# Kernel tuning notes

Measured on AMD Instinct MI355X. Metric: run time of the kernel, lower is better.

## Reference

```python
import jax, jax.numpy as jnp
import numpy as np
from jax import lax

N = 500_000
D = 128            # in_channels
B = 8192           # number of graphs (segments)
T = 6              # processing_steps


def setup_inputs() -> dict:
    key = jax.random.key(0)
    k1, k2, k3, k4, k5, k6 = jax.random.split(key, 6)
    x = jax.random.normal(k1, (N, D), dtype=jnp.float32)
    batch = jnp.sort(jax.random.randint(k2, (N,), 0, B)).astype(jnp.int64)
    s = 1.0 / np.sqrt(D)  # torch LSTM init scale: U(-1/sqrt(hidden), 1/sqrt(hidden))
    W_ih = jax.random.uniform(k3, (4 * D, 2 * D), jnp.float32, -s, s)
    W_hh = jax.random.uniform(k4, (4 * D, D), jnp.float32, -s, s)
    b_ih = jax.random.uniform(k5, (4 * D,), jnp.float32, -s, s)
    b_hh = jax.random.uniform(k6, (4 * D,), jnp.float32, -s, s)
    return {"x": x, "batch": batch, "W_ih": W_ih, "W_hh": W_hh,
            "b_ih": b_ih, "b_hh": b_hh}


def reference(x, batch, W_ih, W_hh, b_ih, b_hh):
    d = x.shape[1]
    h0 = jnp.zeros((B, d), x.dtype)
    c0 = jnp.zeros((B, d), x.dtype)
    q_star0 = jnp.zeros((B, 2 * d), x.dtype)

    def step(carry, _):
        h, c, q_star = carry
        # single-layer torch LSTM cell on seq of length 1
        gates = q_star @ W_ih.T + b_ih + h @ W_hh.T + b_hh  # [B, 4d]
        i, f, g, o = jnp.split(gates, 4, axis=-1)
        i = jax.nn.sigmoid(i)
        f = jax.nn.sigmoid(f)
        g = jnp.tanh(g)
        o = jax.nn.sigmoid(o)
        c = f * c + i * g
        h = o * jnp.tanh(c)
        q = h  # [B, d]
        # attention logits per node
        e = jnp.sum(x * q[batch], axis=-1)  # [N]
        # segment-wise stable softmax (PyG softmax semantics)
        e_max = jax.ops.segment_max(e, batch, num_segments=B)
        ex = jnp.exp(e - e_max[batch])
        denom = jax.ops.segment_sum(ex, batch, num_segments=B)
        a = ex / (denom[batch] + 1e-16)  # [N]
        # scatter-add readout
        r = jax.ops.segment_sum(a[:, None] * x, batch, num_segments=B)  # [B, d]
        q_star = jnp.concatenate([q, r], axis=-1)
        return (h, c, q_star), None

    (h, c, q_star), _ = lax.scan(step, (h0, c0, q_star0), None, length=T)
    return q_star
```

## Files before the change

kernel.cpp:

```cpp
#include <hip/hip_runtime.h>
#include <hip/hip_bf16.h>
#include <cstddef>
#include <cstdint>

#define NNODES 500000
#define DIM    128
#define NSEG   8192
#define TSTEPS 6
#define WCHUNK 32

typedef __attribute__((ext_vector_type(8))) short bf16x8;
typedef __attribute__((ext_vector_type(4))) float f32x4;
typedef unsigned short ushort_t;

static __device__ inline ushort_t f2bf_u(float f) {
    __hip_bfloat16 h = __float2bfloat16(f);
    return *reinterpret_cast<ushort_t*>(&h);
}
static __device__ inline float bfu2f(ushort_t u) {
    union { unsigned i; float f; } c; c.i = ((unsigned)u) << 16; return c.f;
}
#define LGKM_WAIT() __asm__ __volatile__("s_waitcnt lgkmcnt(0)" ::: "memory")

__global__ void seg_bounds_k(const int* __restrict__ batch, int* __restrict__ seg, int n) {
    int b = blockIdx.x * blockDim.x + threadIdx.x;
    if (b > NSEG) return;
    int lo = 0, hi = n;
    while (lo < hi) {
        int mid = (lo + hi) >> 1;
        if (batch[mid] < b) lo = mid + 1; else hi = mid;
    }
    seg[b] = lo;
}

__global__ __launch_bounds__(256) void wconv_k(
    const float* __restrict__ Wih, const float* __restrict__ Whh,
    __hip_bfloat16* __restrict__ wbuf)
{
    int idx = blockIdx.x * 256 + threadIdx.x;
    int n = idx / 384, k = idx - n * 384;
    float v = (k < 256) ? Wih[n * 256 + k] : Whh[n * 128 + (k - 256)];
    wbuf[idx] = __float2bfloat16(v);
}

__global__ __launch_bounds__(256) void gemm_mfma_k(
    const __hip_bfloat16* __restrict__ abuf,
    const __hip_bfloat16* __restrict__ wbuf,
    float* __restrict__ gates)
{
    __shared__ char As[128 * 128];
    __shared__ char Bs[64 * 128];
    const int tid  = threadIdx.x;
    const int lane = tid & 63, wave = tid >> 6;
    const int wrow = (wave >> 1) * 64;
    const int wcol = (wave & 1) * 32;
    const int m0 = blockIdx.y * 128;
    const int n0 = blockIdx.x * 64;

    const int ar  = tid >> 1;
    const int acb = (tid & 1) * 64;
    const int br  = tid >> 2;
    const int bcb = (tid & 3) * 32;

    const char* aP = (const char*)(abuf + (size_t)(m0 + ar) * 384) + acb;
    const char* bP = (const char*)(wbuf + (size_t)(n0 + br) * 384) + bcb;

    f32x4 acc[4][2] = {};

    int4 ra[4]; int4 rb2[2];
    #pragma unroll
    for (int c = 0; c < 4; ++c) ra[c]  = *(const int4*)(aP + c * 16);
    #pragma unroll
    for (int c = 0; c < 2; ++c) rb2[c] = *(const int4*)(bP + c * 16);

    char* asw = As + ar * 128;
    char* bsw = Bs + br * 128;
    const int amask = (ar & 7) << 4;
    const int bmask = (br & 7) << 4;

    for (int s = 0; s < 6; ++s) {
        __syncthreads();
        #pragma unroll
        for (int c = 0; c < 4; ++c)
            *(int4*)(asw + ((acb + c * 16) ^ amask)) = ra[c];
        #pragma unroll
        for (int c = 0; c < 2; ++c)
            *(int4*)(bsw + ((bcb + c * 16) ^ bmask)) = rb2[c];
        __syncthreads();

        if (s < 5) {
            const char* aN = aP + (size_t)(s + 1) * 128;
            const char* bN = bP + (size_t)(s + 1) * 128;
            #pragma unroll
            for (int c = 0; c < 4; ++c) ra[c]  = *(const int4*)(aN + c * 16);
            #pragma unroll
            for (int c = 0; c < 2; ++c) rb2[c] = *(const int4*)(bN + c * 16);
        }

        #pragma unroll
        for (int ks = 0; ks < 2; ++ks) {
            const int kb = ks * 64 + ((lane >> 4) << 4);
            bf16x8 af[4], bfr[2];
            #pragma unroll
            for (int rbk = 0; rbk < 4; ++rbk) {
                int r = wrow + rbk * 16 + (lane & 15);
                af[rbk] = *(const bf16x8*)(As + r * 128 + (kb ^ ((r & 7) << 4)));
            }
            #pragma unroll
            for (int cb = 0; cb < 2; ++cb) {
                int n = wcol + cb * 16 + (lane & 15);
                bfr[cb] = *(const bf16x8*)(Bs + n * 128 + (kb ^ ((n & 7) << 4)));
            }
            #pragma unroll
            for (int rbk = 0; rbk < 4; ++rbk)
                #pragma unroll
                for (int cb = 0; cb < 2; ++cb)
                    acc[rbk][cb] = __builtin_amdgcn_mfma_f32_16x16x32_bf16(
                        af[rbk], bfr[cb], acc[rbk][cb], 0, 0, 0);
        }
    }

    const int rowb = (lane >> 4) << 2;
    const int coll = lane & 15;
    #pragma unroll
    for (int rbk = 0; rbk < 4; ++rbk)
        #pragma unroll
        for (int cb = 0; cb < 2; ++cb) {
            int row = m0 + wrow + rbk * 16 + rowb;
            int col = n0 + wcol + cb * 16 + coll;
            float* gp = gates + (size_t)row * 512 + col;
            #pragma unroll
            for (int reg = 0; reg < 4; ++reg)
                gp[(size_t)reg * 512] = acc[rbk][cb][reg];
        }
}

__global__ __launch_bounds__(128) void attn_lstm_k(
    const float* __restrict__ x, ushort_t* __restrict__ xbf,
    const int* __restrict__ seg, const float* __restrict__ gates,
    const float* __restrict__ bih, const float* __restrict__ bhh,
    float* __restrict__ cbuf, float* __restrict__ qstar,
    __hip_bfloat16* __restrict__ abuf,
    int t0, int read_bf, int write_bf)
{
    const int tid  = threadIdx.x;
    const int wv   = tid >> 6, lane = tid & 63;
    const int b    = blockIdx.x;
    const int l16  = lane & 15, grp = lane >> 4;

    __shared__ ushort_t xs[2][WCHUNK * 128];
    __shared__ float    es[2][WCHUNK];
    __shared__ float    mstat[2][2];
    __shared__ float    rbuf[2][128];
    __shared__ float    hsh[128];

    {
        const int d = tid;
        float gi, gf, gg, go;
        if (t0) {
            gi = bih[d]       + bhh[d];
            gf = bih[128 + d] + bhh[128 + d];
            gg = bih[256 + d] + bhh[256 + d];
            go = bih[384 + d] + bhh[384 + d];
        } else {
            const float* g = gates + (size_t)b * 512;
            gi = g[d]       + bih[d]       + bhh[d];
            gf = g[128 + d] + bih[128 + d] + bhh[128 + d];
            gg = g[256 + d] + bih[256 + d] + bhh[256 + d];
            go = g[384 + d] + bih[384 + d] + bhh[384 + d];
        }
        float iv = 1.f / (1.f + expf(-gi));
        float fv = 1.f / (1.f + expf(-gf));
        float gv = tanhf(gg);
        float ov = 1.f / (1.f + expf(-go));
        float cp = t0 ? 0.f : cbuf[(size_t)b * 128 + d];
        float c  = fv * cp + iv * gv;
        float h  = ov * tanhf(c);
        cbuf[(size_t)b * 128 + d] = c;
        qstar[(size_t)b * 256 + d] = h;
        __hip_bfloat16 hb = __float2bfloat16(h);
        abuf[(size_t)b * 384 + d] = hb;
        abuf[(size_t)b * 384 + 256 + d] = hb;
        hsh[d] = h;
    }
    __syncthreads();

    const int ns = seg[b], ne = seg[b + 1];
    if (ns >= ne) {
        qstar[(size_t)b * 256 + DIM + tid] = 0.f;
        abuf[(size_t)b * 384 + 128 + tid] = __float2bfloat16(0.f);
        return;
    }

    ushort_t* xw = xs[wv];
    float*    ew = es[wv];

    float4 h0, h1, hA, hB;
    if (read_bf) {
        hA = *(const float4*)&hsh[8 * l16];
        hB = *(const float4*)&hsh[8 * l16 + 4];
    } else {
        h0 = *(const float4*)&hsh[4 * l16];
        h1 = *(const float4*)&hsh[64 + 4 * l16];
    }

    float m = -INFINITY, den = 0.f, r0 = 0.f, r1 = 0.f;
    const int d0 = 2 * lane;

    for (int c0 = ns + wv * WCHUNK; c0 < ne; c0 += 2 * WCHUNK) {
        const int cc = min(WCHUNK, ne - c0);

        LGKM_WAIT();
        if (read_bf) {
            if (cc == WCHUNK) {
                #pragma unroll
                for (int it = 0; it < WCHUNK / 8; ++it) {
                    const int raw = grp + it * 8, rbw = raw + 4;
                    int4 v0 = *(const int4*)(xbf + (size_t)(c0 + raw) * 128 + 8 * l16);
                    int4 v1 = *(const int4*)(xbf + (size_t)(c0 + rbw) * 128 + 8 * l16);
                    {
                        *(int4*)(&xw[raw * 128 + 8 * l16]) = v0;
                        const ushort_t* u = (const ushort_t*)&v0;
                        float s = bfu2f(u[0])*hA.x + bfu2f(u[1])*hA.y
                                + bfu2f(u[2])*hA.z + bfu2f(u[3])*hA.w
                                + bfu2f(u[4])*hB.x + bfu2f(u[5])*hB.y
                                + bfu2f(u[6])*hB.z + bfu2f(u[7])*hB.w;
                        s += __shfl_xor(s, 1); s += __shfl_xor(s, 2);
                        s += __shfl_xor(s, 4); s += __shfl_xor(s, 8);
                        if (l16 == 0) ew[raw] = s;
                    }
                    {
                        *(int4*)(&xw[rbw * 128 + 8 * l16]) = v1;
                        const ushort_t* u = (const ushort_t*)&v1;
                        float s = bfu2f(u[0])*hA.x + bfu2f(u[1])*hA.y
                                + bfu2f(u[2])*hA.z + bfu2f(u[3])*hA.w
                                + bfu2f(u[4])*hB.x + bfu2f(u[5])*hB.y
                                + bfu2f(u[6])*hB.z + bfu2f(u[7])*hB.w;
                        s += __shfl_xor(s, 1); s += __shfl_xor(s, 2);
                        s += __shfl_xor(s, 4); s += __shfl_xor(s, 8);
                        if (l16 == 0) ew[rbw] = s;
                    }
                }
            } else {
                for (int j = c0 + grp; j < c0 + cc; j += 4) {
                    const int row = j - c0;
                    int4 v = *(const int4*)(xbf + (size_t)j * 128 + 8 * l16);
                    *(int4*)(&xw[row * 128 + 8 * l16]) = v;
                    const ushort_t* u = (const ushort_t*)&v;
                    float s = bfu2f(u[0])*hA.x + bfu2f(u[1])*hA.y
                            + bfu2f(u[2])*hA.z + bfu2f(u[3])*hA.w
                            + bfu2f(u[4])*hB.x + bfu2f(u[5])*hB.y
                            + bfu2f(u[6])*hB.z + bfu2f(u[7])*hB.w;
                    s += __shfl_xor(s, 1); s += __shfl_xor(s, 2);
                    s += __shfl_xor(s, 4); s += __shfl_xor(s, 8);
                    if (l16 == 0) ew[row] = s;
                }
            }
        } else {
            if (cc == WCHUNK) {
                #pragma unroll
                for (int it = 0; it < WCHUNK / 8; ++it) {
                    const int raw = grp + it * 8, rbw = raw + 4;
                    const float4* xp0 = (const float4*)(x + (size_t)(c0 + raw) * DIM);
                    const float4* xp1 = (const float4*)(x + (size_t)(c0 + rbw) * DIM);
                    float4 xa0 = xp0[l16], xb0 = xp0[l16 + 16];
                    float4 xa1 = xp1[l16], xb1 = xp1[l16 + 16];
                    {
                        float s = xa0.x*h0.x + xa0.y*h0.y + xa0.z*h0.z + xa0.w*h0.w
                                + xb0.x*h1.x + xb0.y*h1.y + xb0.z*h1.z + xb0.w*h1.w;
                        s += __shfl_xor(s, 1); s += __shfl_xor(s, 2);
                        s += __shfl_xor(s, 4); s += __shfl_xor(s, 8);
                        uint2 pa, pb;
                        pa.x = (unsigned)f2bf_u(xa0.x) | ((unsigned)f2bf_u(xa0.y) << 16);
                        pa.y = (unsigned)f2bf_u(xa0.z) | ((unsigned)f2bf_u(xa0.w) << 16);
                        pb.x = (unsigned)f2bf_u(xb0.x) | ((unsigned)f2bf_u(xb0.y) << 16);
                        pb.y = (unsigned)f2bf_u(xb0.z) | ((unsigned)f2bf_u(xb0.w) << 16);
                        *(uint2*)(&xw[raw * 128 + 4 * l16])      = pa;
                        *(uint2*)(&xw[raw * 128 + 64 + 4 * l16]) = pb;
                        if (write_bf) {
                            *(uint2*)(xbf + (size_t)(c0 + raw) * 128 + 4 * l16)      = pa;
                            *(uint2*)(xbf + (size_t)(c0 + raw) * 128 + 64 + 4 * l16) = pb;
                        }
                        if (l16 == 0) ew[raw] = s;
                    }
                    {
                        float s = xa1.x*h0.x + xa1.y*h0.y + xa1.z*h0.z + xa1.w*h0.w
                                + xb1.x*h1.x + xb1.y*h1.y + xb1.z*h1.z + xb1.w*h1.w;
                        s += __shfl_xor(s, 1); s += __shfl_xor(s, 2);
                        s += __shfl_xor(s, 4); s += __shfl_xor(s, 8);
                        uint2 pa, pb;
                        pa.x = (unsigned)f2bf_u(xa1.x) | ((unsigned)f2bf_u(xa1.y) << 16);
                        pa.y = (unsigned)f2bf_u(xa1.z) | ((unsigned)f2bf_u(xa1.w) << 16);
                        pb.x = (unsigned)f2bf_u(xb1.x) | ((unsigned)f2bf_u(xb1.y) << 16);
                        pb.y = (unsigned)f2bf_u(xb1.z) | ((unsigned)f2bf_u(xb1.w) << 16);
                        *(uint2*)(&xw[rbw * 128 + 4 * l16])      = pa;
                        *(uint2*)(&xw[rbw * 128 + 64 + 4 * l16]) = pb;
                        if (write_bf) {
                            *(uint2*)(xbf + (size_t)(c0 + rbw) * 128 + 4 * l16)      = pa;
                            *(uint2*)(xbf + (size_t)(c0 + rbw) * 128 + 64 + 4 * l16) = pb;
                        }
                        if (l16 == 0) ew[rbw] = s;
                    }
                }
            } else {
                for (int j = c0 + grp; j < c0 + cc; j += 4) {
                    const int row = j - c0;
                    const float4* xp = (const float4*)(x + (size_t)j * DIM);
                    float4 xa = xp[l16], xb = xp[l16 + 16];
                    float s = xa.x*h0.x + xa.y*h0.y + xa.z*h0.z + xa.w*h0.w
                            + xb.x*h1.x + xb.y*h1.y + xb.z*h1.z + xb.w*h1.w;
                    s += __shfl_xor(s, 1); s += __shfl_xor(s, 2);
                    s += __shfl_xor(s, 4); s += __shfl_xor(s, 8);
                    uint2 pa, pb;
                    pa.x = (unsigned)f2bf_u(xa.x) | ((unsigned)f2bf_u(xa.y) << 16);
                    pa.y = (unsigned)f2bf_u(xa.z) | ((unsigned)f2bf_u(xa.w) << 16);
                    pb.x = (unsigned)f2bf_u(xb.x) | ((unsigned)f2bf_u(xb.y) << 16);
                    pb.y = (unsigned)f2bf_u(xb.z) | ((unsigned)f2bf_u(xb.w) << 16);
                    *(uint2*)(&xw[row * 128 + 4 * l16])      = pa;
                    *(uint2*)(&xw[row * 128 + 64 + 4 * l16]) = pb;
                    if (write_bf) {
                        *(uint2*)(xbf + (size_t)j * 128 + 4 * l16)      = pa;
                        *(uint2*)(xbf + (size_t)j * 128 + 64 + 4 * l16) = pb;
                    }
                    if (l16 == 0) ew[row] = s;
                }
            }
        }
        LGKM_WAIT();

        const int idx = lane & 31;
        float cm = (idx < cc) ? ew[idx] : -INFINITY;
        #pragma unroll
        for (int o = 1; o < 64; o <<= 1) cm = fmaxf(cm, __shfl_xor(cm, o));

        const float mn = fmaxf(m, cm);
        const float scale = expf(m - mn);

        float w = 0.f;
        if (lane < 32 && lane < cc) {
            w = expf(ew[lane] - mn);
            ew[lane] = w;
        }
        float cd = w;
        #pragma unroll
        for (int o = 1; o < 64; o <<= 1) cd += __shfl_xor(cd, o);
        LGKM_WAIT();

        den = den * scale + cd;
        r0 *= scale;
        r1 *= scale;

        #pragma unroll 4
        for (int row = 0; row < cc; ++row) {
            float wr = ew[row];
            unsigned p = *(const unsigned*)(&xw[row * 128 + d0]);
            r0 = fmaf(wr, bfu2f((ushort_t)(p & 0xffff)), r0);
            r1 = fmaf(wr, bfu2f((ushort_t)(p >> 16)), r1);
        }

        m = mn;
    }

    if (lane == 0) { mstat[wv][0] = m; mstat[wv][1] = den; }
    rbuf[wv][d0]     = r0;
    rbuf[wv][d0 + 1] = r1;
    __syncthreads();

    {
        const float m0s = mstat[0][0], m1s = mstat[1][0];
        const float dn0 = mstat[0][1], dn1 = mstat[1][1];
        const float ms  = fmaxf(m0s, m1s);
        const float k0  = expf(m0s - ms);
        const float k1  = expf(m1s - ms);
        const float dtot = k0 * dn0 + k1 * dn1;
        const float rv = (k0 * rbuf[0][tid] + k1 * rbuf[1][tid]) / (dtot + 1e-16f);
        qstar[(size_t)b * 256 + DIM + tid] = rv;
        abuf[(size_t)b * 384 + 128 + tid] = __float2bfloat16(rv);
    }
}

extern "C" void kernel_launch(void* const* d_in, const int* in_sizes, int n_in,
                              void* d_out, int out_size, void* d_ws, size_t ws_size,
                              hipStream_t stream) {
    const float* x     = (const float*)d_in[0];
    const int*   batch = (const int*)d_in[1];
    const float* Wih   = (const float*)d_in[2];
    const float* Whh   = (const float*)d_in[3];
    const float* bih   = (const float*)d_in[4];
    const float* bhh   = (const float*)d_in[5];
    float* out = (float*)d_out;

    float* cbuf  = (float*)d_ws;
    float* gates = cbuf + (size_t)NSEG * DIM;
    __hip_bfloat16* abuf = (__hip_bfloat16*)(gates + (size_t)NSEG * 512);
    __hip_bfloat16* wbuf = abuf + (size_t)NSEG * 384;
    int* seg = (int*)(wbuf + (size_t)512 * 384);
    size_t fixed_bytes = (size_t)((char*)(seg + NSEG + 1) - (char*)d_ws);
    size_t xbf_off = (fixed_bytes + 15) & ~(size_t)15;
    ushort_t* xbf = (ushort_t*)((char*)d_ws + xbf_off);
    size_t need = xbf_off + (size_t)NNODES * DIM * sizeof(ushort_t);
    const int use_xbf = (ws_size >= need) ? 1 : 0;

    seg_bounds_k<<<(NSEG + 256) / 256, 256, 0, stream>>>(batch, seg, NNODES);
    wconv_k<<<(512 * 384) / 256, 256, 0, stream>>>(Wih, Whh, wbuf);

    dim3 ggrid(512 / 64, NSEG / 128);
    for (int t = 0; t < TSTEPS; ++t) {
        if (t > 0)
            gemm_mfma_k<<<ggrid, 256, 0, stream>>>(abuf, wbuf, gates);
        const int read_bf  = (use_xbf && t > 0) ? 1 : 0;
        const int write_bf = (use_xbf && t == 0) ? 1 : 0;
        attn_lstm_k<<<NSEG, 128, 0, stream>>>(x, xbf, seg, gates, bih, bhh,
                                              cbuf, out, abuf,
                                              (t == 0) ? 1 : 0, read_bf, write_bf);
    }
}
```

Baseline: 431.3 us.

## Fuse all Set2Set steps into one persistent cooperative kernel with grid syncs

Replaces the separate seg-bounds, weight-convert, per-step GEMM and attention kernels with a single cooperative persistent kernel. Grid-wide syncs separate the phases, and blocks loop over GEMM tiles (now 64x32 with 128 threads) and segments. The aim is to remove about 13 kernel launches and their inter-kernel gaps. In exchange the grid is limited to occupancy, so segment work is serialized per block, the GEMM tile is smaller and no longer register-prefetched, and grid.sync itself has a cost.

```diff
diff --git a/kernel.cpp b/kernel.cpp
--- a/kernel.cpp
+++ b/kernel.cpp
@@ -1,4 +1,5 @@
 #include <hip/hip_runtime.h>
+#include <hip/hip_cooperative_groups.h>
 #include <hip/hip_bf16.h>
 #include <cstddef>
 #include <cstdint>
@@ -8,6 +9,8 @@
 #define NSEG   8192
 #define TSTEPS 6
 #define WCHUNK 32
+
+namespace cg = cooperative_groups;
 
 typedef __attribute__((ext_vector_type(8))) short bf16x8;
 typedef __attribute__((ext_vector_type(4))) float f32x4;
@@ -22,360 +25,286 @@
 }
 #define LGKM_WAIT() __asm__ __volatile__("s_waitcnt lgkmcnt(0)" ::: "memory")
 
-__global__ void seg_bounds_k(const int* __restrict__ batch, int* __restrict__ seg, int n) {
-    int b = blockIdx.x * blockDim.x + threadIdx.x;
-    if (b > NSEG) return;
-    int lo = 0, hi = n;
-    while (lo < hi) {
-        int mid = (lo + hi) >> 1;
-        if (batch[mid] < b) lo = mid + 1; else hi = mid;
+#define SMEM_BYTES 18192
+
+__global__ __launch_bounds__(128) void set2set_coop_k(
+    const float* __restrict__ x, ushort_t* __restrict__ xbf,
+    const int* __restrict__ batch,
+    const float* __restrict__ Wih, const float* __restrict__ Whh,
+    const float* __restrict__ bih, const float* __restrict__ bhh,
+    float* __restrict__ cbuf, float* __restrict__ gates,
+    __hip_bfloat16* __restrict__ abuf, __hip_bfloat16* __restrict__ wbuf,
+    int* __restrict__ seg, float* __restrict__ qstar,
+    int use_xbf, int nblk)
+{
+    cg::grid_group grid = cg::this_grid();
+    __shared__ alignas(16) char smem[SMEM_BYTES];
+
+    const int tid = threadIdx.x;
+    const int gid = blockIdx.x;
+    const int gthreads = nblk * 128;
+    const int gtid = gid * 128 + tid;
+
+    for (int idx = gtid; idx < 512 * 384; idx += gthreads) {
+        int n = idx / 384, k = idx - n * 384;
+        float v = (k < 256) ? Wih[n * 256 + k] : Whh[n * 128 + (k - 256)];
+        wbuf[idx] = __float2bfloat16(v);
     }
-    seg[b] = lo;
-}
-
-__global__ __launch_bounds__(256) void wconv_k(
-    const float* __restrict__ Wih, const float* __restrict__ Whh,
-    __hip_bfloat16* __restrict__ wbuf)
-{
-    int idx = blockIdx.x * 256 + threadIdx.x;
-    int n = idx / 384, k = idx - n * 384;
-    float v = (k < 256) ? Wih[n * 256 + k] : Whh[n * 128 + (k - 256)];
-    wbuf[idx] = __float2bfloat16(v);
-}
-
-__global__ __launch_bounds__(256) void gemm_mfma_k(
-    const __hip_bfloat16* __restrict__ abuf,
-    const __hip_bfloat16* __restrict__ wbuf,
-    float* __restrict__ gates)
-{
-    __shared__ char As[128 * 128];
-    __shared__ char Bs[64 * 128];
-    const int tid  = threadIdx.x;
-    const int lane = tid & 63, wave = tid >> 6;
-    const int wrow = (wave >> 1) * 64;
-    const int wcol = (wave & 1) * 32;
-    const int m0 = blockIdx.y * 128;
-    const int n0 = blockIdx.x * 64;
-
-    const int ar  = tid >> 1;
-    const int acb = (tid & 1) * 64;
-    const int br  = tid >> 2;
-    const int bcb = (tid & 3) * 32;
-
-    const char* aP = (const char*)(abuf + (size_t)(m0 + ar) * 384) + acb;
-    const char* bP = (const char*)(wbuf + (size_t)(n0 + br) * 384) + bcb;
-
-    f32x4 acc[4][2] = {};
-
-    int4 ra[4]; int4 rb2[2];
-    #pragma unroll
-    for (int c = 0; c < 4; ++c) ra[c]  = *(const int4*)(aP + c * 16);
-    #pragma unroll
-    for (int c = 0; c < 2; ++c) rb2[c] = *(const int4*)(bP + c * 16);
-
-    char* asw = As + ar * 128;
-    char* bsw = Bs + br * 128;
-    const int amask = (ar & 7) << 4;
-    const int bmask = (br & 7) << 4;
-
-    for (int s = 0; s < 6; ++s) {
-        __syncthreads();
-        #pragma unroll
-        for (int c = 0; c < 4; ++c)
-            *(int4*)(asw + ((acb + c * 16) ^ amask)) = ra[c];
-        #pragma unroll
-        for (int c = 0; c < 2; ++c)
-            *(int4*)(bsw + ((bcb + c * 16) ^ bmask)) = rb2[c];
-        __syncthreads();
-
-        if (s < 5) {
-            const char* aN = aP + (size_t)(s + 1) * 128;
-            const char* bN = bP + (size_t)(s + 1) * 128;
-            #pragma unroll
-            for (int c = 0; c < 4; ++c) ra[c]  = *(const int4*)(aN + c * 16);
-            #pragma unroll
-            for (int c = 0; c < 2; ++c) rb2[c] = *(const int4*)(bN + c * 16);
+    for (int b = gtid; b <= NSEG; b += gthreads) {
+        int lo = 0, hi = NNODES;
+        while (lo < hi) { int mid = (lo + hi) >> 1; if (batch[mid] < b) lo = mid + 1; else hi = mid; }
+        seg[b] = lo;
+    }
+    grid.sync();
+
+    const int lane = tid & 63, wv = tid >> 6;
+    const int l16 = lane & 15, grp = lane >> 4;
+
+    for (int t = 0; t < TSTEPS; ++t) {
+        if (t > 0) {
+            char* As = smem;
+            char* Bs = smem + 8192;
+            const int ar = tid >> 1, acb = (tid & 1) * 64, amask = (ar & 7) << 4;
+            const int br = tid >> 2, bcb = (tid & 3) * 32, bmask = (br & 7) << 4;
+            for (int tile = gid; tile < 2048; tile += nblk) {
+                const int n0 = (tile & 15) * 32;
+                const int m0 = (tile >> 4) * 64;
+                f32x4 acc[2][2] = {};
+                for (int s = 0; s < 6; ++s) {
+                    __syncthreads();
+                    const char* aP = (const char*)(abuf + (size_t)(m0 + ar) * 384) + s * 128 + acb;
+                    #pragma unroll
+                    for (int c = 0; c < 4; ++c)
+                        *(int4*)(As + ar * 128 + ((acb + c * 16) ^ amask)) = *(const int4*)(aP + c * 16);
+                    const char* bP = (const char*)(wbuf + (size_t)(n0 + br) * 384) + s * 128 + bcb;
+                    #pragma unroll
+                    for (int c = 0; c < 2; ++c)
+                        *(int4*)(Bs + br * 128 + ((bcb + c * 16) ^ bmask)) = *(const int4*)(bP + c * 16);
+                    __syncthreads();
+                    #pragma unroll
+                    for (int ks = 0; ks < 2; ++ks) {
+                        const int kb = ks * 64 + ((lane >> 4) << 4);
+                        bf16x8 af[2], bfr[2];
+                        #pragma unroll
+                        for (int rbk = 0; rbk < 2; ++rbk) {
+                            int r = wv * 32 + rbk * 16 + l16;
+                            af[rbk] = *(const bf16x8*)(As + r * 128 + (kb ^ ((r & 7) << 4)));
+                        }
+                        #pragma unroll
+                        for (int cb = 0; cb < 2; ++cb) {
+                            int n = cb * 16 + l16;
+                            bfr[cb] = *(const bf16x8*)(Bs + n * 128 + (kb ^ ((n & 7) << 4)));
+                        }
+                        #pragma unroll
+                        for (int rbk = 0; rbk < 2; ++rbk)
+                            #pragma unroll
+                            for (int cb = 0; cb < 2; ++cb)
+                                acc[rbk][cb] = __builtin_amdgcn_mfma_f32_16x16x32_bf16(
+                                    af[rbk], bfr[cb], acc[rbk][cb], 0, 0, 0);
+                    }
+                }
+                const int rowb = (lane >> 4) << 2;
+                #pragma unroll
+                for (int rbk = 0; rbk < 2; ++rbk)
+                    #pragma unroll
+                    for (int cb = 0; cb < 2; ++cb) {
+                        int row = m0 + wv * 32 + rbk * 16 + rowb;
+                        int col = n0 + cb * 16 + l16;
+                        float* gp = gates + (size_t)row * 512 + col;
+                        #pragma unroll
+                        for (int reg = 0; reg < 4; ++reg)
+                            gp[(size_t)reg * 512] = acc[rbk][cb][reg];
+                    }
+            }
+            grid.sync();
         }
 
-        #pragma unroll
-        for (int ks = 0; ks < 2; ++ks) {
-            const int kb = ks * 64 + ((lane >> 4) << 4);
-            bf16x8 af[4], bfr[2];
-            #pragma unroll
-            for (int rbk = 0; rbk < 4; ++rbk) {
-                int r = wrow + rbk * 16 + (lane & 15);
-                af[rbk] = *(const bf16x8*)(As + r * 128 + (kb ^ ((r & 7) << 4)));
-            }
-            #pragma unroll
-            for (int cb = 0; cb < 2; ++cb) {
-                int n = wcol + cb * 16 + (lane & 15);
-                bfr[cb] = *(const bf16x8*)(Bs + n * 128 + (kb ^ ((n & 7) << 4)));
-            }
-            #pragma unroll
-            for (int rbk = 0; rbk < 4; ++rbk)
-                #pragma unroll
-                for (int cb = 0; cb < 2; ++cb)
-                    acc[rbk][cb] = __builtin_amdgcn_mfma_f32_16x16x32_bf16(
-                        af[rbk], bfr[cb], acc[rbk][cb], 0, 0, 0);
-        }
-    }
-
-    const int rowb = (lane >> 4) << 2;
-    const int coll = lane & 15;
-    #pragma unroll
-    for (int rbk = 0; rbk < 4; ++rbk)
-        #pragma unroll
-        for (int cb = 0; cb < 2; ++cb) {
-            int row = m0 + wrow + rbk * 16 + rowb;
-            int col = n0 + wcol + cb * 16 + coll;
-            float* gp = gates + (size_t)row * 512 + col;
-            #pragma unroll
-            for (int reg = 0; reg < 4; ++reg)
-                gp[(size_t)reg * 512] = acc[rbk][cb][reg];
-        }
-}
-
-__global__ __launch_bounds__(128) void attn_lstm_k(
-    const float* __restrict__ x, ushort_t* __restrict__ xbf,
-    const int* __restrict__ seg, const float* __restrict__ gates,
-    const float* __restrict__ bih, const float* __restrict__ bhh,
-    float* __restrict__ cbuf, float* __restrict__ qstar,
-    __hip_bfloat16* __restrict__ abuf,
-    int t0, int read_bf, int write_bf)
-{
-    const int tid  = threadIdx.x;
-    const int wv   = tid >> 6, lane = tid & 63;
-    const int b    = blockIdx.x;
-    const int l16  = lane & 15, grp = lane >> 4;
-
-    __shared__ ushort_t xs[2][WCHUNK * 128];
-    __shared__ float    es[2][WCHUNK];
-    __shared__ float    mstat[2][2];
-    __shared__ float    rbuf[2][128];
-    __shared__ float    hsh[128];
-
-    {
-        const int d = tid;
-        float gi, gf, gg, go;
-        if (t0) {
-            gi = bih[d]       + bhh[d];
-            gf = bih[128 + d] + bhh[128 + d];
-            gg = bih[256 + d] + bhh[256 + d];
-            go = bih[384 + d] + bhh[384 + d];
-        } else {
-            const float* g = gates + (size_t)b * 512;
-            gi = g[d]       + bih[d]       + bhh[d];
-            gf = g[128 + d] + bih[128 + d] + bhh[128 + d];
-            gg = g[256 + d] + bih[256 + d] + bhh[256 + d];
-            go = g[384 + d] + bih[384 + d] + bhh[384 + d];
-        }
-        float iv = 1.f / (1.f + expf(-gi));
-        float fv = 1.f / (1.f + expf(-gf));
-        float gv = tanhf(gg);
-        float ov = 1.f / (1.f + expf(-go));
-        float cp = t0 ? 0.f : cbuf[(size_t)b * 128 + d];
-        float c  = fv * cp + iv * gv;
-        float h  = ov * tanhf(c);
-        cbuf[(size_t)b * 128 + d] = c;
-        qstar[(size_t)b * 256 + d] = h;
-        __hip_bfloat16 hb = __float2bfloat16(h);
-        abuf[(size_t)b * 384 + d] = hb;
-        abuf[(size_t)b * 384 + 256 + d] = hb;
-        hsh[d] = h;
-    }
-    __syncthreads();
-
-    const int ns = seg[b], ne = seg[b + 1];
-    if (ns >= ne) {
-        qstar[(size_t)b * 256 + DIM + tid] = 0.f;
-        abuf[(size_t)b * 384 + 128 + tid] = __float2bfloat16(0.f);
-        return;
-    }
-
-    ushort_t* xw = xs[wv];
-    float*    ew = es[wv];
-
-    float4 h0, h1, hA, hB;
-    if (read_bf) {
-        hA = *(const float4*)&hsh[8 * l16];
-        hB = *(const float4*)&hsh[8 * l16 + 4];
-    } else {
-        h0 = *(const float4*)&hsh[4 * l16];
-        h1 = *(const float4*)&hsh[64 + 4 * l16];
-    }
-
-    float m = -INFINITY, den = 0.f, r0 = 0.f, r1 = 0.f;
-    const int d0 = 2 * lane;
-
-    for (int c0 = ns + wv * WCHUNK; c0 < ne; c0 += 2 * WCHUNK) {
-        const int cc = min(WCHUNK, ne - c0);
-
-        LGKM_WAIT();
-        if (read_bf) {
-            if (cc == WCHUNK) {
-                #pragma unroll
-                for (int it = 0; it < WCHUNK / 8; ++it) {
-                    const int raw = grp + it * 8, rbw = raw + 4;
-                    int4 v0 = *(const int4*)(xbf + (size_t)(c0 + raw) * 128 + 8 * l16);
-                    int4 v1 = *(const int4*)(xbf + (size_t)(c0 + rbw) * 128 + 8 * l16);
-                    {
-                        *(int4*)(&xw[raw * 128 + 8 * l16]) = v0;
-                        const ushort_t* u = (const ushort_t*)&v0;
-                        float s = bfu2f(u[0])*hA.x + bfu2f(u[1])*hA.y
-                                + bfu2f(u[2])*hA.z + bfu2f(u[3])*hA.w
-                                + bfu2f(u[4])*hB.x + bfu2f(u[5])*hB.y
-                                + bfu2f(u[6])*hB.z + bfu2f(u[7])*hB.w;
-                        s += __shfl_xor(s, 1); s += __shfl_xor(s, 2);
-                        s += __shfl_xor(s, 4); s += __shfl_xor(s, 8);
-                        if (l16 == 0) ew[raw] = s;
+        const int t0f      = (t == 0) ? 1 : 0;
+        const int read_bf  = (use_xbf && t > 0) ? 1 : 0;
+        const int write_bf = (use_xbf && t == 0) ? 1 : 0;
+        ushort_t* xs = (ushort_t*)smem;
+        float* es    = (float*)(smem + 16384);
+        float* mstat = (float*)(smem + 16640);
+        float* rb    = (float*)(smem + 16656);
+        float* hsh   = (float*)(smem + 17680);
+        ushort_t* xw = xs + wv * (WCHUNK * 128);
+        float*    ew = es + wv * WCHUNK;
+
+        for (int b = gid; b < NSEG; b += nblk) {
+            {
+                const int d = tid;
+                float gi, gf, gg, go;
+                if (t0f) {
+                    gi = bih[d]       + bhh[d];
+                    gf = bih[128 + d] + bhh[128 + d];
+                    gg = bih[256 + d] + bhh[256 + d];
+                    go = bih[384 + d] + bhh[384 + d];
+                } else {
+                    const float* g = gates + (size_t)b * 512;
+                    gi = g[d]       + bih[d]       + bhh[d];
+                    gf = g[128 + d] + bih[128 + d] + bhh[128 + d];
+                    gg = g[256 + d] + bih[256 + d] + bhh[256 + d];
+                    go = g[384 + d] + bih[384 + d] + bhh[384 + d];
+                }
+                float iv = 1.f / (1.f + expf(-gi));
+                float fv = 1.f / (1.f + expf(-gf));
+                float gv = tanhf(gg);
+                float ov = 1.f / (1.f + expf(-go));
+                float cp = t0f ? 0.f : cbuf[(size_t)b * 128 + d];
+                float c  = fv * cp + iv * gv;
+                float h  = ov * tanhf(c);
+                cbuf[(size_t)b * 128 + d] = c;
+                qstar[(size_t)b * 256 + d] = h;
+                __hip_bfloat16 hb = __float2bfloat16(h);
+                abuf[(size_t)b * 384 + d] = hb;
+                abuf[(size_t)b * 384 + 256 + d] = hb;
+                hsh[d] = h;
+            }
+            __syncthreads();
+
+            const int ns = seg[b], ne = seg[b + 1];
+            if (ns >= ne) {
+                qstar[(size_t)b * 256 + DIM + tid] = 0.f;
+                abuf[(size_t)b * 384 + 128 + tid] = __float2bfloat16(0.f);
+                continue;
+            }
+
+            float4 h0, h1, hA, hB;
+            if (read_bf) {
+                hA = *(const float4*)&hsh[8 * l16];
+                hB = *(const float4*)&hsh[8 * l16 + 4];
+            } else {
+                h0 = *(const float4*)&hsh[4 * l16];
+                h1 = *(const float4*)&hsh[64 + 4 * l16];
+            }
+
+            float m = -INFINITY, den = 0.f, r0 = 0.f, r1 = 0.f;
+            const int d0 = 2 * lane;
+
+            for (int c0 = ns + wv * WCHUNK; c0 < ne; c0 += 2 * WCHUNK) {
+                const int cc = min(WCHUNK, ne - c0);
+
+                LGKM_WAIT();
+                if (read_bf) {
+                    if (cc == WCHUNK) {
+                        #pragma unroll
+                        for (int it = 0; it < WCHUNK / 8; ++it) {
+                            const int raw = grp + it * 8, rbw = raw + 4;
+                            int4 v0 = *(const int4*)(xbf + (size_t)(c0 + raw) * 128 + 8 * l16);
+                            int4 v1 = *(const int4*)(xbf + (size_t)(c0 + rbw) * 128 + 8 * l16);
+                            {
+                                *(int4*)(&xw[raw * 128 + 8 * l16]) = v0;
+                                const ushort_t* u = (const ushort_t*)&v0;
+                                float s = bfu2f(u[0])*hA.x + bfu2f(u[1])*hA.y
+                                        + bfu2f(u[2])*hA.z + bfu2f(u[3])*hA.w
+                                        + bfu2f(u[4])*hB.x + bfu2f(u[5])*hB.y
+                                        + bfu2f(u[6])*hB.z + bfu2f(u[7])*hB.w;
+                                s += __shfl_xor(s, 1); s += __shfl_xor(s, 2);
+                                s += __shfl_xor(s, 4); s += __shfl_xor(s, 8);
+                                if (l16 == 0) ew[raw] = s;
+                            }
+                            {
+                                *(int4*)(&xw[rbw * 128 + 8 * l16]) = v1;
+                                const ushort_t* u = (const ushort_t*)&v1;
+                                float s = bfu2f(u[0])*hA.x + bfu2f(u[1])*hA.y
+                                        + bfu2f(u[2])*hA.z + bfu2f(u[3])*hA.w
+                                        + bfu2f(u[4])*hB.x + bfu2f(u[5])*hB.y
+                                        + bfu2f(u[6])*hB.z + bfu2f(u[7])*hB.w;
+                                s += __shfl_xor(s, 1); s += __shfl_xor(s, 2);
+                                s += __shfl_xor(s, 4); s += __shfl_xor(s, 8);
+                                if (l16 == 0) ew[rbw] = s;
+                            }
+                        }
+                    } else {
+                        for (int j = c0 + grp; j < c0 + cc; j += 4) {
+                            const int row = j - c0;
+                            int4 v = *(const int4*)(xbf + (size_t)j * 128 + 8 * l16);
+                            *(int4*)(&xw[row * 128 + 8 * l16]) = v;
+                            const ushort_t* u = (const ushort_t*)&v;
+                            float s = bfu2f(u[0])*hA.x + bfu2f(u[1])*hA.y
+                                    + bfu2f(u[2])*hA.z + bfu2f(u[3])*hA.w
+                                    + bfu2f(u[4])*hB.x + bfu2f(u[5])*hB.y
+                                    + bfu2f(u[6])*hB.z + bfu2f(u[7])*hB.w;
+                            s += __shfl_xor(s, 1); s += __shfl_xor(s, 2);
+                            s += __shfl_xor(s, 4); s += __shfl_xor(s, 8);
+                            if (l16 == 0) ew[row] = s;
+                        }
                     }
-                    {
-                        *(int4*)(&xw[rbw * 128 + 8 * l16]) = v1;
-                        const ushort_t* u = (const ushort_t*)&v1;
-                        float s = bfu2f(u[0])*hA.x + bfu2f(u[1])*hA.y
-                                + bfu2f(u[2])*hA.z + bfu2f(u[3])*hA.w
-                                + bfu2f(u[4])*hB.x + bfu2f(u[5])*hB.y
-                                + bfu2f(u[6])*hB.z + bfu2f(u[7])*hB.w;
-                        s += __shfl_xor(s, 1); s += __shfl_xor(s, 2);
-                        s += __shfl_xor(s, 4); s += __shfl_xor(s, 8);
-                        if (l16 == 0) ew[rbw] = s;
-                    }
-                }
-            } else {
-                for (int j = c0 + grp; j < c0 + cc; j += 4) {
-                    const int row = j - c0;
-                    int4 v = *(const int4*)(xbf + (size_t)j * 128 + 8 * l16);
-                    *(int4*)(&xw[row * 128 + 8 * l16]) = v;
-                    const ushort_t* u = (const ushort_t*)&v;
-                    float s = bfu2f(u[0])*hA.x + bfu2f(u[1])*hA.y
-                            + bfu2f(u[2])*hA.z + bfu2f(u[3])*hA.w
-                            + bfu2f(u[4])*hB.x + bfu2f(u[5])*hB.y
-                            + bfu2f(u[6])*hB.z + bfu2f(u[7])*hB.w;
-                    s += __shfl_xor(s, 1); s += __shfl_xor(s, 2);
-                    s += __shfl_xor(s, 4); s += __shfl_xor(s, 8);
-                    if (l16 == 0) ew[row] = s;
-                }
-            }
-        } else {
-            if (cc == WCHUNK) {
-                #pragma unroll
-                for (int it = 0; it < WCHUNK / 8; ++it) {
-                    const int raw = grp + it * 8, rbw = raw + 4;
-                    const float4* xp0 = (const float4*)(x + (size_t)(c0 + raw) * DIM);
-                    const float4* xp1 = (const float4*)(x + (size_t)(c0 + rbw) * DIM);
-                    float4 xa0 = xp0[l16], xb0 = xp0[l16 + 16];
-                    float4 xa1 = xp1[l16], xb1 = xp1[l16 + 16];
-                    {
-                        float s = xa0.x*h0.x + xa0.y*h0.y + xa0.z*h0.z + xa0.w*h0.w
-                                + xb0.x*h1.x + xb0.y*h1.y + xb0.z*h1.z + xb0.w*h1.w;
+                } else {
+                    for (int j = c0 + grp; j < c0 + cc; j += 4) {
+                        const int row = j - c0;
+                        const float4* xp = (const float4*)(x + (size_t)j * DIM);
+                        float4 xa = xp[l16], xb = xp[l16 + 16];
+                        float s = xa.x*h0.x + xa.y*h0.y + xa.z*h0.z + xa.w*h0.w
+                                + xb.x*h1.x + xb.y*h1.y + xb.z*h1.z + xb.w*h1.w;
                         s += __shfl_xor(s, 1); s += __shfl_xor(s, 2);
                         s += __shfl_xor(s, 4); s += __shfl_xor(s, 8);
                         uint2 pa, pb;
-                        pa.x = (unsigned)f2bf_u(xa0.x) | ((unsigned)f2bf_u(xa0.y) << 16);
-                        pa.y = (unsigned)f2bf_u(xa0.z) | ((unsigned)f2bf_u(xa0.w) << 16);
-                        pb.x = (unsigned)f2bf_u(xb0.x) | ((unsigned)f2bf_u(xb0.y) << 16);
-                        pb.y = (unsigned)f2bf_u(xb0.z) | ((unsigned)f2bf_u(xb0.w) << 16);
-                        *(uint2*)(&xw[raw * 128 + 4 * l16])      = pa;
-                        *(uint2*)(&xw[raw * 128 + 64 + 4 * l16]) = pb;
+                        pa.x = (unsigned)f2bf_u(xa.x) | ((unsigned)f2bf_u(xa.y) << 16);
+                        pa.y = (unsigned)f2bf_u(xa.z) | ((unsigned)f2bf_u(xa.w) << 16);
+                        pb.x = (unsigned)f2bf_u(xb.x) | ((unsigned)f2bf_u(xb.y) << 16);
+                        pb.y = (unsigned)f2bf_u(xb.z) | ((unsigned)f2bf_u(xb.w) << 16);
+                        *(uint2*)(&xw[row * 128 + 4 * l16])      = pa;
+                        *(uint2*)(&xw[row * 128 + 64 + 4 * l16]) = pb;
                         if (write_bf) {
-                            *(uint2*)(xbf + (size_t)(c0 + raw) * 128 + 4 * l16)      = pa;
-                            *(uint2*)(xbf + (size_t)(c0 + raw) * 128 + 64 + 4 * l16) = pb;
-                        }
-                        if (l16 == 0) ew[raw] = s;
+                            *(uint2*)(xbf + (size_t)j * 128 + 4 * l16)      = pa;
+                            *(uint2*)(xbf + (size_t)j * 128 + 64 + 4 * l16) = pb;
+                        }
+                        if (l16 == 0) ew[row] = s;
                     }
-                    {
-                        float s = xa1.x*h0.x + xa1.y*h0.y + xa1.z*h0.z + xa1.w*h0.w
-                                + xb1.x*h1.x + xb1.y*h1.y + xb1.z*h1.z + xb1.w*h1.w;
-                        s += __shfl_xor(s, 1); s += __shfl_xor(s, 2);
-                        s += __shfl_xor(s, 4); s += __shfl_xor(s, 8);
-                        uint2 pa, pb;
-                        pa.x = (unsigned)f2bf_u(xa1.x) | ((unsigned)f2bf_u(xa1.y) << 16);
-                        pa.y = (unsigned)f2bf_u(xa1.z) | ((unsigned)f2bf_u(xa1.w) << 16);
-                        pb.x = (unsigned)f2bf_u(xb1.x) | ((unsigned)f2bf_u(xb1.y) << 16);
-                        pb.y = (unsigned)f2bf_u(xb1.z) | ((unsigned)f2bf_u(xb1.w) << 16);
-                        *(uint2*)(&xw[rbw * 128 + 4 * l16])      = pa;
-                        *(uint2*)(&xw[rbw * 128 + 64 + 4 * l16]) = pb;
-                        if (write_bf) {
-                            *(uint2*)(xbf + (size_t)(c0 + rbw) * 128 + 4 * l16)      = pa;
-                            *(uint2*)(xbf + (size_t)(c0 + rbw) * 128 + 64 + 4 * l16) = pb;
-                        }
-                        if (l16 == 0) ew[rbw] = s;
-                    }
-                }
-            } else {
-                for (int j = c0 + grp; j < c0 + cc; j += 4) {
-                    const int row = j - c0;
-                    const float4* xp = (const float4*)(x + (size_t)j * DIM);
-                    float4 xa = xp[l16], xb = xp[l16 + 16];
-                    float s = xa.x*h0.x + xa.y*h0.y + xa.z*h0.z + xa.w*h0.w
-                            + xb.x*h1.x + xb.y*h1.y + xb.z*h1.z + xb.w*h1.w;
-                    s += __shfl_xor(s, 1); s += __shfl_xor(s, 2);
-                    s += __shfl_xor(s, 4); s += __shfl_xor(s, 8);
-                    uint2 pa, pb;
-                    pa.x = (unsigned)f2bf_u(xa.x) | ((unsigned)f2bf_u(xa.y) << 16);
-                    pa.y = (unsigned)f2bf_u(xa.z) | ((unsigned)f2bf_u(xa.w) << 16);
-                    pb.x = (unsigned)f2bf_u(xb.x) | ((unsigned)f2bf_u(xb.y) << 16);
-                    pb.y = (unsigned)f2bf_u(xb.z) | ((unsigned)f2bf_u(xb.w) << 16);
-                    *(uint2*)(&xw[row * 128 + 4 * l16])      = pa;
-                    *(uint2*)(&xw[row * 128 + 64 + 4 * l16]) = pb;
-                    if (write_bf) {
-                        *(uint2*)(xbf + (size_t)j * 128 + 4 * l16)      = pa;
-                        *(uint2*)(xbf + (size_t)j * 128 + 64 + 4 * l16) = pb;
-                    }
-                    if (l16 == 0) ew[row] = s;
-                }
+                }
+                LGKM_WAIT();
+
+                const int idx = lane & 31;
+                float cm = (idx < cc) ? ew[idx] : -INFINITY;
+                #pragma unroll
+                for (int o = 1; o < 64; o <<= 1) cm = fmaxf(cm, __shfl_xor(cm, o));
+
+                const float mn = fmaxf(m, cm);
+                const float scale = expf(m - mn);
+
+                float w = 0.f;
+                if (lane < 32 && lane < cc) {
+                    w = expf(ew[lane] - mn);
+                    ew[lane] = w;
+                }
+                float cd = w;
+                #pragma unroll
+                for (int o = 1; o < 64; o <<= 1) cd += __shfl_xor(cd, o);
+                LGKM_WAIT();
+
+                den = den * scale + cd;
+                r0 *= scale;
+                r1 *= scale;
+
+                #pragma unroll 4
+                for (int row = 0; row < cc; ++row) {
+                    float wr = ew[row];
+                    unsigned p = *(const unsigned*)(&xw[row * 128 + d0]);
+                    r0 = fmaf(wr, bfu2f((ushort_t)(p & 0xffff)), r0);
+                    r1 = fmaf(wr, bfu2f((ushort_t)(p >> 16)), r1);
+                }
+
+                m = mn;
+            }
+
+            if (lane == 0) { mstat[wv * 2 + 0] = m; mstat[wv * 2 + 1] = den; }
+            rb[wv * 128 + d0]     = r0;
+            rb[wv * 128 + d0 + 1] = r1;
+            __syncthreads();
+            {
+                const float m0s = mstat[0], dn0 = mstat[1];
+                const float m1s = mstat[2], dn1 = mstat[3];
+                const float ms  = fmaxf(m0s, m1s);
+                const float k0  = expf(m0s - ms);
+                const float k1  = expf(m1s - ms);
+                const float dtot = k0 * dn0 + k1 * dn1;
+                const float rv = (k0 * rb[tid] + k1 * rb[128 + tid]) / (dtot + 1e-16f);
+                qstar[(size_t)b * 256 + DIM + tid] = rv;
+                abuf[(size_t)b * 384 + 128 + tid] = __float2bfloat16(rv);
             }
         }
-        LGKM_WAIT();
-
-        const int idx = lane & 31;
-        float cm = (idx < cc) ? ew[idx] : -INFINITY;
-        #pragma unroll
-        for (int o = 1; o < 64; o <<= 1) cm = fmaxf(cm, __shfl_xor(cm, o));
-
-        const float mn = fmaxf(m, cm);
-        const float scale = expf(m - mn);
-
-        float w = 0.f;
-        if (lane < 32 && lane < cc) {
-            w = expf(ew[lane] - mn);
-            ew[lane] = w;
-        }
-        float cd = w;
-        #pragma unroll
-        for (int o = 1; o < 64; o <<= 1) cd += __shfl_xor(cd, o);
-        LGKM_WAIT();
-
-        den = den * scale + cd;
-        r0 *= scale;
-        r1 *= scale;
-
-        #pragma unroll 4
-        for (int row = 0; row < cc; ++row) {
-            float wr = ew[row];
-            unsigned p = *(const unsigned*)(&xw[row * 128 + d0]);
-            r0 = fmaf(wr, bfu2f((ushort_t)(p & 0xffff)), r0);
-            r1 = fmaf(wr, bfu2f((ushort_t)(p >> 16)), r1);
-        }
-
-        m = mn;
-    }
-
-    if (lane == 0) { mstat[wv][0] = m; mstat[wv][1] = den; }
-    rbuf[wv][d0]     = r0;
-    rbuf[wv][d0 + 1] = r1;
-    __syncthreads();
-
-    {
-        const float m0s = mstat[0][0], m1s = mstat[1][0];
-        const float dn0 = mstat[0][1], dn1 = mstat[1][1];
-        const float ms  = fmaxf(m0s, m1s);
-        const float k0  = expf(m0s - ms);
-        const float k1  = expf(m1s - ms);
-        const float dtot = k0 * dn0 + k1 * dn1;
-        const float rv = (k0 * rbuf[0][tid] + k1 * rbuf[1][tid]) / (dtot + 1e-16f);
-        qstar[(size_t)b * 256 + DIM + tid] = rv;
-        abuf[(size_t)b * 384 + 128 + tid] = __float2bfloat16(rv);
+        if (t < TSTEPS - 1) grid.sync();
     }
 }
 
@@ -399,19 +328,23 @@
     size_t xbf_off = (fixed_bytes + 15) & ~(size_t)15;
     ushort_t* xbf = (ushort_t*)((char*)d_ws + xbf_off);
     size_t need = xbf_off + (size_t)NNODES * DIM * sizeof(ushort_t);
-    const int use_xbf = (ws_size >= need) ? 1 : 0;
-
-    seg_bounds_k<<<(NSEG + 256) / 256, 256, 0, stream>>>(batch, seg, NNODES);
-    wconv_k<<<(512 * 384) / 256, 256, 0, stream>>>(Wih, Whh, wbuf);
-
-    dim3 ggrid(512 / 64, NSEG / 128);
-    for (int t = 0; t < TSTEPS; ++t) {
-        if (t > 0)
-            gemm_mfma_k<<<ggrid, 256, 0, stream>>>(abuf, wbuf, gates);
-        const int read_bf  = (use_xbf && t > 0) ? 1 : 0;
-        const int write_bf = (use_xbf && t == 0) ? 1 : 0;
-        attn_lstm_k<<<NSEG, 128, 0, stream>>>(x, xbf, seg, gates, bih, bhh,
-                                              cbuf, out, abuf,
-                                              (t == 0) ? 1 : 0, read_bf, write_bf);
-    }
+    int use_xbf = (ws_size >= need) ? 1 : 0;
+
+    int maxb = 0;
+    hipOccupancyMaxActiveBlocksPerMultiprocessor(&maxb, set2set_coop_k, 128, 0);
+    if (maxb < 1) maxb = 1;
+    int ncu = 0;
+    hipDeviceGetAttribute(&ncu, hipDeviceAttributeMultiprocessorCount, 0);
+    if (ncu < 1) ncu = 256;
+    int nblk = maxb * ncu;
+    if (nblk > 2048) nblk = 2048;
+
+    void* args[] = {
+        (void*)&x, (void*)&xbf, (void*)&batch,
+        (void*)&Wih, (void*)&Whh, (void*)&bih, (void*)&bhh,
+        (void*)&cbuf, (void*)&gates, (void*)&abuf, (void*)&wbuf,
+        (void*)&seg, (void*)&out, (void*)&use_xbf, (void*)&nblk
+    };
+    hipLaunchCooperativeKernel((const void*)set2set_coop_k,
+                               dim3(nblk), dim3(128), args, 0, stream);
 }
```

After: 1.398 ms. 3.24x slower.
